# Kernel optimization log

Measured on AMD Instinct MI355X. Metric: run time of the kernel, lower is better.

## Reference

```python
import jax, jax.numpy as jnp
import numpy as np

ATT_TIMES = 2
EPS = 1e-12  # torch F.normalize eps

N_NODES = 200000
EMB_DIM = 256
ATT_NUM = 2


def setup_inputs() -> dict:
    key = jax.random.key(0)
    k1, k2 = jax.random.split(key)
    x = jax.random.normal(k1, (N_NODES, EMB_DIM), dtype=jnp.float32)
    # glorot/xavier-normal init for the att_num projection matrices W_i
    std = float(np.sqrt(2.0 / (EMB_DIM + EMB_DIM)))
    W = jax.random.normal(k2, (ATT_NUM, EMB_DIM, EMB_DIM), dtype=jnp.float32) * std
    return {"x": x, "W": W}


def _one_attention(x, Wi):
    """One attention head (att_style='dot', att_weight=True), iterated ATT_TIMES."""
    xi = x
    out = None
    for _ in range(ATT_TIMES):
        temp = jnp.mean(xi, axis=0, keepdims=True)          # (1, D)
        h_avg = jnp.tanh(temp @ Wi)                          # (1, D)
        # 'dot' style: interact with W = identity -> scores = x @ h_avg^T, (N, 1)
        scores = xi @ h_avg.T                                # (N, 1)
        # F.normalize(p=1, dim=1) on an (N,1) column: divide by max(|v|, eps)
        norm = jnp.maximum(jnp.sum(jnp.abs(scores), axis=1, keepdims=True), EPS)
        att = jax.nn.sigmoid(scores / norm)                  # (N, 1)
        out = att.T @ xi                                     # (1, D)
        xi = xi * att                                        # re-weight for next round
    return out


def reference(x, W):
    att_num = W.shape[0]
    outs = [_one_attention(x, W[i]) for i in range(att_num)]
    return jnp.concatenate(outs, axis=1)                     # (1, att_num * D)
```

## Files before the change

kernel.cpp:

```cpp
#include <hip/hip_runtime.h>
#include <math.h>

#define NROWS 200000
#define D 256
#define F4 64

#define NBLK 500
#define CHUNK 400
#define ITERS 25

#define WS_H1 0
#define WS_H2 512
#define WS_A  1024
#define WS_P1 401024
#define WS_P2 529024
#define WS_XB 785024

__device__ __forceinline__ float att_sigmoid(float s) {
    float t = s / fmaxf(fabsf(s), 1e-12f);
    return 1.0f / (1.0f + __expf(-t));
}

__device__ __forceinline__ unsigned int packbf2(float a, float b) {
    unsigned int ua = __float_as_uint(a);
    unsigned int ub = __float_as_uint(b);
    ua = (ua + 0x7FFFu + ((ua >> 16) & 1u)) >> 16;
    ub = (ub + 0x7FFFu + ((ub >> 16) & 1u)) >> 16;
    return ua | (ub << 16);
}

__device__ __forceinline__ void unpack8(uint4 q, float* f) {
    f[0] = __uint_as_float(q.x << 16); f[1] = __uint_as_float(q.x & 0xFFFF0000u);
    f[2] = __uint_as_float(q.y << 16); f[3] = __uint_as_float(q.y & 0xFFFF0000u);
    f[4] = __uint_as_float(q.z << 16); f[5] = __uint_as_float(q.z & 0xFFFF0000u);
    f[6] = __uint_as_float(q.w << 16); f[7] = __uint_as_float(q.w & 0xFFFF0000u);
}

__global__ void __launch_bounds__(256) colsum_cast_kernel(const float* __restrict__ x,
                                                          float* __restrict__ part,
                                                          uint2* __restrict__ xb2) {
    const int tid = threadIdx.x, lane = tid & 63, wv = tid >> 6;
    const float4* x4 = reinterpret_cast<const float4*>(x);
    const int r0 = blockIdx.x * CHUNK + wv * 4;
    const size_t base = (size_t)r0 * F4 + lane;
    float4 cur[4], nxt[4];
#pragma unroll
    for (int j = 0; j < 4; ++j) cur[j] = x4[base + j * F4];
    float4 accA = make_float4(0.f, 0.f, 0.f, 0.f);
    float4 accB = make_float4(0.f, 0.f, 0.f, 0.f);
    for (int it = 0; it < ITERS; ++it) {
        if (it + 1 < ITERS) {
            size_t nb = base + (size_t)(it + 1) * 16 * F4;
#pragma unroll
            for (int j = 0; j < 4; ++j) nxt[j] = x4[nb + j * F4];
        }
        accA.x += cur[0].x + cur[1].x; accB.x += cur[2].x + cur[3].x;
        accA.y += cur[0].y + cur[1].y; accB.y += cur[2].y + cur[3].y;
        accA.z += cur[0].z + cur[1].z; accB.z += cur[2].z + cur[3].z;
        accA.w += cur[0].w + cur[1].w; accB.w += cur[2].w + cur[3].w;
        const int rb = r0 + it * 16;
#pragma unroll
        for (int j = 0; j < 4; ++j) {
            xb2[(size_t)(rb + j) * 64 + lane] =
                make_uint2(packbf2(cur[j].x, cur[j].y), packbf2(cur[j].z, cur[j].w));
        }
        if (it + 1 < ITERS) {
#pragma unroll
            for (int j = 0; j < 4; ++j) cur[j] = nxt[j];
        }
    }
    accA.x += accB.x; accA.y += accB.y; accA.z += accB.z; accA.w += accB.w;
    __shared__ float4 sh[256];
    sh[tid] = accA;
    __syncthreads();
    if (tid < 64) {
        float4 a = sh[tid], b = sh[tid + 64], c = sh[tid + 128], d = sh[tid + 192];
        float4 s;
        s.x = (a.x + b.x) + (c.x + d.x);
        s.y = (a.y + b.y) + (c.y + d.y);
        s.z = (a.z + b.z) + (c.z + d.z);
        s.w = (a.w + b.w) + (c.w + d.w);
        reinterpret_cast<float4*>(part)[blockIdx.x * 64 + tid] = s;
    }
}

__global__ void __launch_bounds__(256) hproj_fused(const float* __restrict__ W,
                                                   const float* __restrict__ part,
                                                   int width4, int headOff4, float scale,
                                                   float* __restrict__ hout) {
    const int head = blockIdx.x;
    const int tid = threadIdx.x, lane = tid & 63, wv = tid >> 6;
    const float4* p4 = reinterpret_cast<const float4*>(part) + head * headOff4 + lane;
    float4 s = make_float4(0.f, 0.f, 0.f, 0.f);
#pragma unroll 5
    for (int r = wv; r < NBLK; r += 4) {
        float4 v = p4[(size_t)r * width4];
        s.x += v.x; s.y += v.y; s.z += v.z; s.w += v.w;
    }
    __shared__ float4 red[4][64];
    __shared__ float vbuf[D];
    red[wv][lane] = s;
    __syncthreads();
    if (tid < 64) {
        float4 a = red[0][tid], b = red[1][tid], c = red[2][tid], d = red[3][tid];
        vbuf[tid * 4 + 0] = ((a.x + b.x) + (c.x + d.x)) * scale;
        vbuf[tid * 4 + 1] = ((a.y + b.y) + (c.y + d.y)) * scale;
        vbuf[tid * 4 + 2] = ((a.z + b.z) + (c.z + d.z)) * scale;
        vbuf[tid * 4 + 3] = ((a.w + b.w) + (c.w + d.w)) * scale;
    }
    __syncthreads();
    const float* Wh = W + head * D * D;
    float acc = 0.0f;
#pragma unroll 8
    for (int k = 0; k < D; ++k) acc = fmaf(vbuf[k], Wh[k * D + tid], acc);
    hout[head * D + tid] = tanhf(acc);
}

__global__ void __launch_bounds__(256) pass1_bf16_kernel(const uint4* __restrict__ xb,
                                                         float* __restrict__ ws) {
    const float* h = ws + WS_H1;
    float* aA0 = ws + WS_A;
    float* aA1 = ws + WS_A + NROWS;
    float* part = ws + WS_P2;
    const int tid = threadIdx.x, lane = tid & 63, wv = tid >> 6;
    const int hi = lane >> 5, chunk = lane & 31, c0 = chunk * 8;
    const int r0 = blockIdx.x * CHUNK + wv * 4;
    float hh0[8], hh1[8];
#pragma unroll
    for (int k = 0; k < 8; ++k) { hh0[k] = h[c0 + k]; hh1[k] = h[D + c0 + k]; }
    float acc0[8], acc1[8];
#pragma unroll
    for (int k = 0; k < 8; ++k) { acc0[k] = 0.f; acc1[k] = 0.f; }
    const size_t base = (size_t)r0 * 32;
    uint4 cur0 = xb[base + lane];
    uint4 cur1 = xb[base + 64 + lane];
    for (int it = 0; it < ITERS; ++it) {
        uint4 nxt0, nxt1;
        if (it + 1 < ITERS) {
            const size_t nb = base + (size_t)(it + 1) * 512;
            nxt0 = xb[nb + lane];
            nxt1 = xb[nb + 64 + lane];
        }
        float f0[8], f1[8];
        unpack8(cur0, f0);
        unpack8(cur1, f1);
        float d00 = 0.f, d01 = 0.f, d10 = 0.f, d11 = 0.f;
#pragma unroll
        for (int k = 0; k < 8; ++k) {
            d00 = fmaf(f0[k], hh0[k], d00); d10 = fmaf(f0[k], hh1[k], d10);
            d01 = fmaf(f1[k], hh0[k], d01); d11 = fmaf(f1[k], hh1[k], d11);
        }
#pragma unroll
        for (int off = 1; off < 32; off <<= 1) {
            d00 += __shfl_xor(d00, off); d01 += __shfl_xor(d01, off);
            d10 += __shfl_xor(d10, off); d11 += __shfl_xor(d11, off);
        }
        float a00 = att_sigmoid(d00), a01 = att_sigmoid(d01);
        float a10 = att_sigmoid(d10), a11 = att_sigmoid(d11);
        const int rb = r0 + it * 16;
        if (chunk == 0) {
            aA0[rb + hi] = a00; aA0[rb + 2 + hi] = a01;
            aA1[rb + hi] = a10; aA1[rb + 2 + hi] = a11;
        }
#pragma unroll
        for (int k = 0; k < 8; ++k) {
            acc0[k] = fmaf(a00, f0[k], acc0[k]); acc0[k] = fmaf(a01, f1[k], acc0[k]);
            acc1[k] = fmaf(a10, f0[k], acc1[k]); acc1[k] = fmaf(a11, f1[k], acc1[k]);
        }
        cur0 = nxt0; cur1 = nxt1;
    }
    __shared__ float lds[256][17];
#pragma unroll
    for (int k = 0; k < 8; ++k) { lds[tid][k] = acc0[k]; lds[tid][8 + k] = acc1[k]; }
    __syncthreads();
    float s0 = 0.f, s1 = 0.f;
#pragma unroll
    for (int g = 0; g < 8; ++g) {
        s0 += lds[g * 32 + (tid >> 3)][tid & 7];
        s1 += lds[g * 32 + (tid >> 3)][8 + (tid & 7)];
    }
    part[blockIdx.x * 512 + tid] = s0;
    part[blockIdx.x * 512 + 256 + tid] = s1;
}

__global__ void __launch_bounds__(256) pass2_bf16_kernel(const uint4* __restrict__ xb,
                                                         float* __restrict__ ws) {
    const float* h = ws + WS_H2;
    const float* aA0 = ws + WS_A;
    const float* aA1 = ws + WS_A + NROWS;
    float* part = ws + WS_P2;
    const int tid = threadIdx.x, lane = tid & 63, wv = tid >> 6;
    const int hi = lane >> 5, chunk = lane & 31, c0 = chunk * 8;
    const int r0 = blockIdx.x * CHUNK + wv * 4;
    float hh0[8], hh1[8];
#pragma unroll
    for (int k = 0; k < 8; ++k) { hh0[k] = h[c0 + k]; hh1[k] = h[D + c0 + k]; }
    float acc0[8], acc1[8];
#pragma unroll
    for (int k = 0; k < 8; ++k) { acc0[k] = 0.f; acc1[k] = 0.f; }
    const size_t base = (size_t)r0 * 32;
    uint4 cur0 = xb[base + lane];
    uint4 cur1 = xb[base + 64 + lane];
    for (int it = 0; it < ITERS; ++it) {
        uint4 nxt0, nxt1;
        if (it + 1 < ITERS) {
            const size_t nb = base + (size_t)(it + 1) * 512;
            nxt0 = xb[nb + lane];
            nxt1 = xb[nb + 64 + lane];
        }
        const int rb = r0 + it * 16;
        float aa00 = aA0[rb + hi], aa01 = aA0[rb + 2 + hi];
        float aa10 = aA1[rb + hi], aa11 = aA1[rb + 2 + hi];
        float f0[8], f1[8];
        unpack8(cur0, f0);
        unpack8(cur1, f1);
        float d00 = 0.f, d01 = 0.f, d10 = 0.f, d11 = 0.f;
#pragma unroll
        for (int k = 0; k < 8; ++k) {
            d00 = fmaf(f0[k], hh0[k], d00); d10 = fmaf(f0[k], hh1[k], d10);
            d01 = fmaf(f1[k], hh0[k], d01); d11 = fmaf(f1[k], hh1[k], d11);
        }
#pragma unroll
        for (int off = 1; off < 32; off <<= 1) {
            d00 += __shfl_xor(d00, off); d01 += __shfl_xor(d01, off);
            d10 += __shfl_xor(d10, off); d11 += __shfl_xor(d11, off);
        }
        float w00 = att_sigmoid(aa00 * d00) * aa00;
        float w01 = att_sigmoid(aa01 * d01) * aa01;
        float w10 = att_sigmoid(aa10 * d10) * aa10;
        float w11 = att_sigmoid(aa11 * d11) * aa11;
#pragma unroll
        for (int k = 0; k < 8; ++k) {
            acc0[k] = fmaf(w00, f0[k], acc0[k]); acc0[k] = fmaf(w01, f1[k], acc0[k]);
            acc1[k] = fmaf(w10, f0[k], acc1[k]); acc1[k] = fmaf(w11, f1[k], acc1[k]);
        }
        cur0 = nxt0; cur1 = nxt1;
    }
    __shared__ float lds[256][17];
#pragma unroll
    for (int k = 0; k < 8; ++k) { lds[tid][k] = acc0[k]; lds[tid][8 + k] = acc1[k]; }
    __syncthreads();
    float s0 = 0.f, s1 = 0.f;
#pragma unroll
    for (int g = 0; g < 8; ++g) {
        s0 += lds[g * 32 + (tid >> 3)][tid & 7];
        s1 += lds[g * 32 + (tid >> 3)][8 + (tid & 7)];
    }
    part[blockIdx.x * 512 + tid] = s0;
    part[blockIdx.x * 512 + 256 + tid] = s1;
}

__global__ void __launch_bounds__(256) out_reduce(const float* __restrict__ part,
                                                  float* __restrict__ out) {
    const int head = blockIdx.x;
    const int tid = threadIdx.x, lane = tid & 63, wv = tid >> 6;
    const float4* p4 = reinterpret_cast<const float4*>(part) + head * 64 + lane;
    float4 s = make_float4(0.f, 0.f, 0.f, 0.f);
#pragma unroll 5
    for (int r = wv; r < NBLK; r += 4) {
        float4 v = p4[(size_t)r * 128];
        s.x += v.x; s.y += v.y; s.z += v.z; s.w += v.w;
    }
    __shared__ float4 red[4][64];
    red[wv][lane] = s;
    __syncthreads();
    if (tid < 64) {
        float4 a = red[0][tid], b = red[1][tid], c = red[2][tid], d = red[3][tid];
        float4 o;
        o.x = (a.x + b.x) + (c.x + d.x);
        o.y = (a.y + b.y) + (c.y + d.y);
        o.z = (a.z + b.z) + (c.z + d.z);
        o.w = (a.w + b.w) + (c.w + d.w);
        reinterpret_cast<float4*>(out)[head * 64 + tid] = o;
    }
}

extern "C" void kernel_launch(void* const* d_in, const int* in_sizes, int n_in,
                              void* d_out, int out_size, void* d_ws, size_t ws_size,
                              hipStream_t stream) {
    const float* x = (const float*)d_in[0];
    const float* W = (const float*)d_in[1];
    float* out = (float*)d_out;
    float* ws = (float*)d_ws;

    uint2* xb2 = reinterpret_cast<uint2*>(ws + WS_XB);
    const uint4* xb4 = reinterpret_cast<const uint4*>(ws + WS_XB);

    colsum_cast_kernel<<<dim3(NBLK), dim3(256), 0, stream>>>(x, ws + WS_P1, xb2);
    hproj_fused<<<dim3(2), dim3(256), 0, stream>>>(W, ws + WS_P1, 64, 0, 1.0f / NROWS, ws + WS_H1);
    pass1_bf16_kernel<<<dim3(NBLK), dim3(256), 0, stream>>>(xb4, ws);
    hproj_fused<<<dim3(2), dim3(256), 0, stream>>>(W, ws + WS_P2, 128, 64, 1.0f / NROWS, ws + WS_H2);
    pass2_bf16_kernel<<<dim3(NBLK), dim3(256), 0, stream>>>(xb4, ws);
    out_reduce<<<dim3(2), dim3(256), 0, stream>>>(ws + WS_P2, out);
}
```

Baseline: 158.0 us.

## Store attention signs as bytes and split passes into more, smaller blocks

```diff
diff --git a/kernel.cpp b/kernel.cpp
--- a/kernel.cpp
+++ b/kernel.cpp
@@ -7,14 +7,16 @@
 
 #define NBLK 500
 #define CHUNK 400
-#define ITERS 25
+#define CITERS 25
+#define NBLK2 1250
+#define CHUNK2 160
+#define PITERS 10
 
 #define WS_H1 0
 #define WS_H2 512
 #define WS_A  1024
-#define WS_P1 401024
-#define WS_P2 529024
-#define WS_XB 785024
+#define WS_P  101024
+#define WS_XB 741024
 
 __device__ __forceinline__ float att_sigmoid(float s) {
     float t = s / fmaxf(fabsf(s), 1e-12f);
@@ -48,8 +50,8 @@
     for (int j = 0; j < 4; ++j) cur[j] = x4[base + j * F4];
     float4 accA = make_float4(0.f, 0.f, 0.f, 0.f);
     float4 accB = make_float4(0.f, 0.f, 0.f, 0.f);
-    for (int it = 0; it < ITERS; ++it) {
-        if (it + 1 < ITERS) {
+    for (int it = 0; it < CITERS; ++it) {
+        if (it + 1 < CITERS) {
             size_t nb = base + (size_t)(it + 1) * 16 * F4;
 #pragma unroll
             for (int j = 0; j < 4; ++j) nxt[j] = x4[nb + j * F4];
@@ -64,7 +66,7 @@
             xb2[(size_t)(rb + j) * 64 + lane] =
                 make_uint2(packbf2(cur[j].x, cur[j].y), packbf2(cur[j].z, cur[j].w));
         }
-        if (it + 1 < ITERS) {
+        if (it + 1 < CITERS) {
 #pragma unroll
             for (int j = 0; j < 4; ++j) cur[j] = nxt[j];
         }
@@ -86,14 +88,14 @@
 
 __global__ void __launch_bounds__(256) hproj_fused(const float* __restrict__ W,
                                                    const float* __restrict__ part,
-                                                   int width4, int headOff4, float scale,
-                                                   float* __restrict__ hout) {
+                                                   int width4, int headOff4, int nparts,
+                                                   float scale, float* __restrict__ hout) {
     const int head = blockIdx.x;
     const int tid = threadIdx.x, lane = tid & 63, wv = tid >> 6;
     const float4* p4 = reinterpret_cast<const float4*>(part) + head * headOff4 + lane;
     float4 s = make_float4(0.f, 0.f, 0.f, 0.f);
 #pragma unroll 5
-    for (int r = wv; r < NBLK; r += 4) {
+    for (int r = wv; r < nparts; r += 4) {
         float4 v = p4[(size_t)r * width4];
         s.x += v.x; s.y += v.y; s.z += v.z; s.w += v.w;
     }
@@ -119,12 +121,12 @@
 __global__ void __launch_bounds__(256) pass1_bf16_kernel(const uint4* __restrict__ xb,
                                                          float* __restrict__ ws) {
     const float* h = ws + WS_H1;
-    float* aA0 = ws + WS_A;
-    float* aA1 = ws + WS_A + NROWS;
-    float* part = ws + WS_P2;
+    unsigned char* aB0 = reinterpret_cast<unsigned char*>(ws + WS_A);
+    unsigned char* aB1 = aB0 + NROWS;
+    float* part = ws + WS_P;
     const int tid = threadIdx.x, lane = tid & 63, wv = tid >> 6;
     const int hi = lane >> 5, chunk = lane & 31, c0 = chunk * 8;
-    const int r0 = blockIdx.x * CHUNK + wv * 4;
+    const int r0 = blockIdx.x * CHUNK2 + wv * 4;
     float hh0[8], hh1[8];
 #pragma unroll
     for (int k = 0; k < 8; ++k) { hh0[k] = h[c0 + k]; hh1[k] = h[D + c0 + k]; }
@@ -134,9 +136,9 @@
     const size_t base = (size_t)r0 * 32;
     uint4 cur0 = xb[base + lane];
     uint4 cur1 = xb[base + 64 + lane];
-    for (int it = 0; it < ITERS; ++it) {
+    for (int it = 0; it < PITERS; ++it) {
         uint4 nxt0, nxt1;
-        if (it + 1 < ITERS) {
+        if (it + 1 < PITERS) {
             const size_t nb = base + (size_t)(it + 1) * 512;
             nxt0 = xb[nb + lane];
             nxt1 = xb[nb + 64 + lane];
@@ -159,8 +161,10 @@
         float a10 = att_sigmoid(d10), a11 = att_sigmoid(d11);
         const int rb = r0 + it * 16;
         if (chunk == 0) {
-            aA0[rb + hi] = a00; aA0[rb + 2 + hi] = a01;
-            aA1[rb + hi] = a10; aA1[rb + 2 + hi] = a11;
+            aB0[rb + hi] = (d00 >= 0.f);
+            aB0[rb + 2 + hi] = (d01 >= 0.f);
+            aB1[rb + hi] = (d10 >= 0.f);
+            aB1[rb + 2 + hi] = (d11 >= 0.f);
         }
 #pragma unroll
         for (int k = 0; k < 8; ++k) {
@@ -186,12 +190,13 @@
 __global__ void __launch_bounds__(256) pass2_bf16_kernel(const uint4* __restrict__ xb,
                                                          float* __restrict__ ws) {
     const float* h = ws + WS_H2;
-    const float* aA0 = ws + WS_A;
-    const float* aA1 = ws + WS_A + NROWS;
-    float* part = ws + WS_P2;
+    const unsigned char* aB0 = reinterpret_cast<const unsigned char*>(ws + WS_A);
+    const unsigned char* aB1 = aB0 + NROWS;
+    float* part = ws + WS_P;
     const int tid = threadIdx.x, lane = tid & 63, wv = tid >> 6;
     const int hi = lane >> 5, chunk = lane & 31, c0 = chunk * 8;
-    const int r0 = blockIdx.x * CHUNK + wv * 4;
+    const int r0 = blockIdx.x * CHUNK2 + wv * 4;
+    const float SIG[2] = {att_sigmoid(-1.0f), att_sigmoid(1.0f)};
     float hh0[8], hh1[8];
 #pragma unroll
     for (int k = 0; k < 8; ++k) { hh0[k] = h[c0 + k]; hh1[k] = h[D + c0 + k]; }
@@ -201,16 +206,16 @@
     const size_t base = (size_t)r0 * 32;
     uint4 cur0 = xb[base + lane];
     uint4 cur1 = xb[base + 64 + lane];
-    for (int it = 0; it < ITERS; ++it) {
+    for (int it = 0; it < PITERS; ++it) {
         uint4 nxt0, nxt1;
-        if (it + 1 < ITERS) {
+        if (it + 1 < PITERS) {
             const size_t nb = base + (size_t)(it + 1) * 512;
             nxt0 = xb[nb + lane];
             nxt1 = xb[nb + 64 + lane];
         }
         const int rb = r0 + it * 16;
-        float aa00 = aA0[rb + hi], aa01 = aA0[rb + 2 + hi];
-        float aa10 = aA1[rb + hi], aa11 = aA1[rb + 2 + hi];
+        float aa00 = SIG[aB0[rb + hi]], aa01 = SIG[aB0[rb + 2 + hi]];
+        float aa10 = SIG[aB1[rb + hi]], aa11 = SIG[aB1[rb + 2 + hi]];
         float f0[8], f1[8];
         unpack8(cur0, f0);
         unpack8(cur1, f1);
@@ -257,7 +262,7 @@
     const float4* p4 = reinterpret_cast<const float4*>(part) + head * 64 + lane;
     float4 s = make_float4(0.f, 0.f, 0.f, 0.f);
 #pragma unroll 5
-    for (int r = wv; r < NBLK; r += 4) {
+    for (int r = wv; r < NBLK2; r += 4) {
         float4 v = p4[(size_t)r * 128];
         s.x += v.x; s.y += v.y; s.z += v.z; s.w += v.w;
     }
@@ -286,10 +291,12 @@
     uint2* xb2 = reinterpret_cast<uint2*>(ws + WS_XB);
     const uint4* xb4 = reinterpret_cast<const uint4*>(ws + WS_XB);
 
-    colsum_cast_kernel<<<dim3(NBLK), dim3(256), 0, stream>>>(x, ws + WS_P1, xb2);
-    hproj_fused<<<dim3(2), dim3(256), 0, stream>>>(W, ws + WS_P1, 64, 0, 1.0f / NROWS, ws + WS_H1);
-    pass1_bf16_kernel<<<dim3(NBLK), dim3(256), 0, stream>>>(xb4, ws);
-    hproj_fused<<<dim3(2), dim3(256), 0, stream>>>(W, ws + WS_P2, 128, 64, 1.0f / NROWS, ws + WS_H2);
-    pass2_bf16_kernel<<<dim3(NBLK), dim3(256), 0, stream>>>(xb4, ws);
-    out_reduce<<<dim3(2), dim3(256), 0, stream>>>(ws + WS_P2, out);
-}
+    colsum_cast_kernel<<<dim3(NBLK), dim3(256), 0, stream>>>(x, ws + WS_P, xb2);
+    hproj_fused<<<dim3(2), dim3(256), 0, stream>>>(W, ws + WS_P, 64, 0, NBLK,
+                                                   1.0f / NROWS, ws + WS_H1);
+    pass1_bf16_kernel<<<dim3(NBLK2), dim3(256), 0, stream>>>(xb4, ws);
+    hproj_fused<<<dim3(2), dim3(256), 0, stream>>>(W, ws + WS_P, 128, 64, NBLK2,
+                                                   1.0f / NROWS, ws + WS_H2);
+    pass2_bf16_kernel<<<dim3(NBLK2), dim3(256), 0, stream>>>(xb4, ws);
+    out_reduce<<<dim3(2), dim3(256), 0, stream>>>(ws + WS_P, out);
+}
```

After: 182.7 us. 1.16x slower.
